# Kernel optimization log

Hardware: AMD Instinct MI355X
Metric: run time of the kernel (lower is better)

## Reference

```python
import jax, jax.numpy as jnp
import numpy as np

V, D, T_BLK, H, HS = 50257, 512, 2048, 8, 64
B, T = 2, 2048


def setup_inputs() -> dict:
    key = jax.random.key(0)
    ks = jax.random.split(key, 12)
    s = 0.02
    return {
        "idx": jax.random.randint(ks[0], (B, T), 0, V),
        "targets": jax.random.randint(ks[1], (B, T), 0, V),
        "tok_emb": jax.random.normal(ks[2], (V, D), jnp.float32) * s,
        "pos_emb": jax.random.normal(ks[3], (T_BLK, D), jnp.float32) * s,
        "wq": jax.random.normal(ks[4], (H, D, HS), jnp.float32) * s,
        "wk": jax.random.normal(ks[5], (H, D, HS), jnp.float32) * s,
        "wv": jax.random.normal(ks[6], (H, D, HS), jnp.float32) * s,
        "w1": jax.random.normal(ks[7], (D, D), jnp.float32) * s,
        "b1": jnp.zeros((D,), jnp.float32),
        "w_head": jax.random.normal(ks[8], (D, V), jnp.float32) * s,
        "b_head": jnp.zeros((V,), jnp.float32),
    }


def _forward(idx, targets, tok_emb, pos_emb, wq, wk, wv, w1, b1, w_head, b_head):
    b, t = idx.shape
    x = tok_emb[idx] + pos_emb[:t]                        # [B,T,D]
    # batched per-head QKV (equivalent to the per-head Linear loop)
    q = jnp.einsum("btd,hde->bhte", x, wq)                # [B,H,T,hs]
    k = jnp.einsum("btd,hde->bhte", x, wk)
    v = jnp.einsum("btd,hde->bhte", x, wv)
    scores = jnp.einsum("bhte,bhse->bhts", q, k) / jnp.sqrt(jnp.float32(HS))
    causal = jnp.tril(jnp.ones((t, t), bool))
    scores = jnp.where(causal, scores, -jnp.inf)
    weights = jax.nn.softmax(scores, axis=-1)
    att = jnp.einsum("bhts,bhse->bhte", weights, v)       # [B,H,T,hs]
    att = att.transpose(0, 2, 1, 3).reshape(b, t, H * HS)  # head-concat order
    x_ff = jax.nn.relu(att @ w1 + b1)                      # [B,T,D]
    logits = x_ff @ w_head + b_head                        # [B,T,V]
    logp = jax.nn.log_softmax(logits, axis=-1)
    loss = -jnp.mean(jnp.take_along_axis(logp, targets[..., None], axis=-1))
    return logits, loss


def reference(idx, targets, tok_emb, pos_emb, wq, wk, wv, w1, b1, w_head, b_head):
    return _forward(idx, targets, tok_emb, pos_emb, wq, wk, wv, w1, b1, w_head, b_head)
```

## Files before the change

### kernel.cpp

```cpp
#include <hip/hip_runtime.h>
#include <hip/hip_bf16.h>
#include <hip/hip_fp8.h>
#include <stdint.h>

#define V_SZ   50257
#define NPAD   50432
#define NT_HEAD 197
#define D_SZ   512
#define HS_SZ  64
#define H_N    8
#define T_SZ   2048
#define ROWS   4096

typedef __bf16 bf16x8 __attribute__((ext_vector_type(8)));
typedef __bf16 bf16x4 __attribute__((ext_vector_type(4)));
typedef float  f32x4  __attribute__((ext_vector_type(4)));
typedef long   l64x2  __attribute__((ext_vector_type(2)));

__device__ __forceinline__ unsigned char to_fp8(float x) {
  __hip_fp8_e4m3 t(x);
  return t.__x;
}

__device__ __forceinline__ void gload_lds16(const void* g, void* l) {
  auto gp = (const __attribute__((address_space(1))) uint32_t*)(uintptr_t)g;
  auto lp = (__attribute__((address_space(3))) uint32_t*)(uintptr_t)l;
  __builtin_amdgcn_global_load_lds(gp, lp, 16, 0, 0);
}

__global__ __launch_bounds__(256) void k_embed(const int* __restrict__ idx,
    const float* __restrict__ tok, const float* __restrict__ pos,
    __bf16* __restrict__ xb) {
  const int row = blockIdx.x;
  const int tpos = row & (T_SZ - 1);
  const int tokid = idx[row];
  const int d = threadIdx.x * 2;
  float2 tv = *(const float2*)(tok + (size_t)tokid * D_SZ + d);
  float2 pv = *(const float2*)(pos + (size_t)tpos * D_SZ + d);
  __bf16* o = xb + (size_t)row * D_SZ + d;
  o[0] = (__bf16)(tv.x + pv.x);
  o[1] = (__bf16)(tv.y + pv.y);
}

__global__ __launch_bounds__(256) void k_prep_wqkv(const float* __restrict__ wq,
    const float* __restrict__ wk, const float* __restrict__ wv, __bf16* __restrict__ dst) {
  const int id = blockIdx.x * 256 + threadIdx.x;
  const int n = id >> 9, dd = id & 511;
  const int mi = n >> 9, rem = n & 511, h = rem >> 6, e = rem & 63;
  const float* src = (mi == 0) ? wq : ((mi == 1) ? wk : wv);
  dst[id] = (__bf16)src[((size_t)h * D_SZ + dd) * HS_SZ + e];
}

__global__ __launch_bounds__(256) void k_prep_w1(const float* __restrict__ w1,
                                                 __bf16* __restrict__ dst) {
  const int id = blockIdx.x * 256 + threadIdx.x;
  const int n = id >> 9, kk = id & 511;
  dst[id] = (__bf16)w1[(size_t)kk * D_SZ + n];
}

__global__ void k_prep_wh(const float* __restrict__ wh, unsigned char* __restrict__ dst) {
  __shared__ float tile[32][33];
  const int n0 = blockIdx.x * 32, d0 = blockIdx.y * 32;
  const int tx = threadIdx.x, ty = threadIdx.y;
  #pragma unroll
  for (int i = 0; i < 4; ++i) {
    int dd = d0 + ty + i * 8, n = n0 + tx;
    tile[ty + i * 8][tx] = (n < V_SZ) ? wh[(size_t)dd * V_SZ + n] : 0.f;
  }
  __syncthreads();
  #pragma unroll
  for (int i = 0; i < 4; ++i) {
    int n = n0 + ty + i * 8, dd = d0 + tx;
    dst[(size_t)n * D_SZ + dd] = to_fp8(tile[tx][ty + i * 8] * 256.f);
  }
}

template <int EPI>
__global__ __launch_bounds__(256) void k_gemm(const __bf16* __restrict__ A,
    const __bf16* __restrict__ Bt, const float* __restrict__ bias,
    unsigned char* __restrict__ outA8, __bf16* __restrict__ outK, __bf16* __restrict__ outV) {
  __shared__ __bf16 As[128 * 32];
  __shared__ __bf16 Bs[128 * 32];
  const int t = threadIdx.x, lane = t & 63, w = t >> 6;
  const int wr = w >> 1, wc = w & 1;
  const int m0 = blockIdx.x * 128, n0 = blockIdx.y * 128;
  const int srow = lane >> 2, k8 = (lane & 3) * 8;

  f32x4 zero = {0.f, 0.f, 0.f, 0.f};
  f32x4 acc[4][4];
  #pragma unroll
  for (int mm = 0; mm < 4; ++mm)
    #pragma unroll
    for (int nn = 0; nn < 4; ++nn) acc[mm][nn] = zero;

  const __bf16* Ag = A  + (size_t)(m0 + w * 16 + srow) * D_SZ + k8;
  const __bf16* Bg = Bt + (size_t)(n0 + w * 16 + srow) * D_SZ + k8;
  char* AsB = (char*)As + w * 1024;
  char* BsB = (char*)Bs + w * 1024;
  const int kslot = (lane >> 4) * 8;
  const int arow = wr * 64 + (lane & 15);
  const int brow = wc * 64 + (lane & 15);

  for (int kt = 0; kt < 16; ++kt) {
    const int k0 = kt * 32;
    gload_lds16(Ag + k0,             AsB);
    gload_lds16(Ag + 64 * D_SZ + k0, AsB + 4096);
    gload_lds16(Bg + k0,             BsB);
    gload_lds16(Bg + 64 * D_SZ + k0, BsB + 4096);
    __syncthreads();

    bf16x8 af[4], bfr[4];
    #pragma unroll
    for (int mm = 0; mm < 4; ++mm)
      af[mm] = *(const bf16x8*)(As + (arow + mm * 16) * 32 + kslot);
    #pragma unroll
    for (int nn = 0; nn < 4; ++nn)
      bfr[nn] = *(const bf16x8*)(Bs + (brow + nn * 16) * 32 + kslot);
    #pragma unroll
    for (int mm = 0; mm < 4; ++mm)
      #pragma unroll
      for (int nn = 0; nn < 4; ++nn)
        acc[mm][nn] = __builtin_amdgcn_mfma_f32_16x16x32_bf16(af[mm], bfr[nn], acc[mm][nn], 0, 0, 0);
    __syncthreads();
  }

  const int lrow = (lane >> 4) * 4, lcol = lane & 15;
  #pragma unroll
  for (int mm = 0; mm < 4; ++mm) {
    #pragma unroll
    for (int nn = 0; nn < 4; ++nn) {
      const int grow0 = m0 + wr * 64 + mm * 16 + lrow;
      const int gcol  = n0 + wc * 64 + nn * 16 + lcol;
      if (EPI == 0) {
        const int mi = gcol >> 9, rem = gcol & 511, hh = rem >> 6, e = rem & 63;
        const int bb = grow0 >> 11, tt0 = grow0 & 2047;
        const int bhh = bb * H_N + hh;
        if (mi == 2) {
          bf16x4 pk = { (__bf16)acc[mm][nn][0], (__bf16)acc[mm][nn][1],
                        (__bf16)acc[mm][nn][2], (__bf16)acc[mm][nn][3] };
          *(bf16x4*)(outV + ((size_t)bhh * HS_SZ + e) * T_SZ + tt0) = pk;
        } else {
          __bf16* dq = (mi == 0 ? (__bf16*)outA8 : outK) + ((size_t)bhh * T_SZ + tt0) * HS_SZ + e;
          const float sc = (mi == 0) ? 0.125f : 1.f;
          #pragma unroll
          for (int j = 0; j < 4; ++j) dq[(size_t)j * HS_SZ] = (__bf16)(acc[mm][nn][j] * sc);
        }
      } else {
        #pragma unroll
        for (int j = 0; j < 4; ++j) {
          float xv = acc[mm][nn][j] + bias[gcol];
          xv = (xv > 0.f ? xv : 0.f) * 256.f;
          outA8[(size_t)(grow0 + j) * D_SZ + gcol] = to_fp8(xv);
        }
      }
    }
  }
}

__global__ __launch_bounds__(512, 4) void k_ghead(const unsigned char* __restrict__ A,
    const unsigned char* __restrict__ Bt, const float* __restrict__ bias,
    float* __restrict__ logits, float2* __restrict__ part) {
  __shared__ char lds[49152];
  const int t = threadIdx.x, lane = t & 63, w = t >> 6;
  const int wr = w >> 2, wc = w & 3;
  const int m0 = blockIdx.x * 128, n0 = blockIdx.y * 256;
  const int lm = lane & 15, g = lane >> 4;
  const int r2 = lane >> 2, c2 = lane & 3;
  const int csw2 = (c2 ^ ((r2 >> 1) & 3)) << 4;

  f32x4 acc[4][4];
  #pragma unroll
  for (int mm = 0; mm < 4; ++mm)
    #pragma unroll
    for (int nn = 0; nn < 4; ++nn) acc[mm][nn] = f32x4{0.f, 0.f, 0.f, 0.f};

  const unsigned char* Ab = A  + (size_t)m0 * D_SZ;
  const unsigned char* Bb = Bt + (size_t)n0 * D_SZ;

  auto STAGE = [&](int buf, int kt) {
    char* Al = lds + buf * 24576;
    char* Bl = Al + 8192;
    gload_lds16(Ab + (size_t)(w * 16 + r2) * D_SZ + kt * 64 + csw2,        Al + w * 1024);
    gload_lds16(Bb + (size_t)(w * 16 + r2) * D_SZ + kt * 64 + csw2,        Bl + w * 1024);
    gload_lds16(Bb + (size_t)(128 + w * 16 + r2) * D_SZ + kt * 64 + csw2,  Bl + 8192 + w * 1024);
  };

  STAGE(0, 0);
  STAGE(1, 1);
  asm volatile("s_waitcnt vmcnt(3)" ::: "memory");
  __builtin_amdgcn_s_barrier();
  asm volatile("" ::: "memory");

  for (int kt = 0; kt < 8; ++kt) {
    const char* Al = lds + (kt & 1) * 24576;
    const char* Bl = Al + 8192;
    l64x2 b2[4];
    #pragma unroll
    for (int nn = 0; nn < 4; ++nn) {
      const int row = wc * 64 + nn * 16 + lm;
      b2[nn] = *(const l64x2*)(Bl + row * 64 + ((g ^ ((row >> 1) & 3)) << 4));
    }
    #pragma unroll
    for (int mm = 0; mm < 4; ++mm) {
      const int row = wr * 64 + mm * 16 + lm;
      l64x2 a2 = *(const l64x2*)(Al + row * 64 + ((g ^ ((row >> 1) & 3)) << 4));
      #pragma unroll
      for (int nn = 0; nn < 4; ++nn)
        acc[mm][nn] = __builtin_amdgcn_mfma_f32_16x16x32_fp8_fp8(a2.x, b2[nn].x, acc[mm][nn], 0, 0, 0);
      #pragma unroll
      for (int nn = 0; nn < 4; ++nn)
        acc[mm][nn] = __builtin_amdgcn_mfma_f32_16x16x32_fp8_fp8(a2.y, b2[nn].y, acc[mm][nn], 0, 0, 0);
    }
    if (kt == 7) break;
    __builtin_amdgcn_s_barrier();
    asm volatile("" ::: "memory");
    if (kt < 6) {
      STAGE(kt & 1, kt + 2);
      asm volatile("s_waitcnt vmcnt(3)" ::: "memory");
    } else {
      asm volatile("s_waitcnt vmcnt(0)" ::: "memory");
    }
    __builtin_amdgcn_s_barrier();
    asm volatile("" ::: "memory");
  }
  __syncthreads();

  const float SC = 1.f / 65536.f;
  float* tr   = (float*)lds;
  float* redS = tr + 32 * 260;
  const int colL = wc * 64 + lm;
  float bj[4]; int vok[4];
  #pragma unroll
  for (int nn = 0; nn < 4; ++nn) {
    const int gc = n0 + colL + nn * 16;
    vok[nn] = (gc < V_SZ);
    bj[nn] = vok[nn] ? bias[gc] : 0.f;
  }
  const int r32s = t >> 4, c16 = t & 15;
  #pragma unroll
  for (int mm = 0; mm < 4; ++mm) {
    if (mm) __syncthreads();
    float sj[4];
    #pragma unroll
    for (int j = 0; j < 4; ++j) {
      const int r32 = wr * 16 + g * 4 + j;
      float s = 0.f;
      #pragma unroll
      for (int nn = 0; nn < 4; ++nn) {
        const float v = acc[mm][nn][j] * SC + bj[nn];
        tr[r32 * 260 + colL + nn * 16] = v;
        if (vok[nn]) s += __expf(v);
      }
      sj[j] = s;
    }
    #pragma unroll
    for (int j = 0; j < 4; ++j) {
      float s = sj[j];
      s += __shfl_xor(s, 1); s += __shfl_xor(s, 2);
      s += __shfl_xor(s, 4); s += __shfl_xor(s, 8);
      if (lm == 0) redS[(wr * 64 + mm * 16 + g * 4 + j) * 4 + wc] = s;
    }
    __syncthreads();
    const int grow = m0 + (r32s >> 4) * 64 + mm * 16 + (r32s & 15);
    float* gp = logits + (size_t)grow * V_SZ;
    #pragma unroll
    for (int i = 0; i < 4; ++i) {
      const int c4 = c16 + 16 * i;
      const int gc0 = n0 + c4 * 4;
      f32x4 vv = *(const f32x4*)(tr + r32s * 260 + c4 * 4);
      if (gc0 + 3 < V_SZ) {
        *(f32x4*)(gp + gc0) = vv;
      } else {
        if (gc0     < V_SZ) gp[gc0]     = vv.x;
        if (gc0 + 1 < V_SZ) gp[gc0 + 1] = vv.y;
        if (gc0 + 2 < V_SZ) gp[gc0 + 2] = vv.z;
        if (gc0 + 3 < V_SZ) gp[gc0 + 3] = vv.w;
      }
    }
  }
  __syncthreads();
  if (t < 128) {
    const float S = redS[t * 4] + redS[t * 4 + 1] + redS[t * 4 + 2] + redS[t * 4 + 3];
    part[(size_t)(m0 + t) * NT_HEAD + blockIdx.y] = float2{0.f, S};
  }
}

__global__ __launch_bounds__(256) void k_attn(const __bf16* __restrict__ qbf,
    const __bf16* __restrict__ kbf, const __bf16* __restrict__ vbf,
    __bf16* __restrict__ xatt) {
  const int qt = 31 - blockIdx.x;
  const int bh = blockIdx.y;
  const int b = bh >> 3, h = bh & 7;
  const int t = threadIdx.x, lane = t & 63, w = t >> 6;
  const int qr = lane & 15, g = lane >> 4, r7 = qr & 7;
  __shared__ __bf16 Klds[64 * 64];
  __shared__ __bf16 Vt[64 * 64];
  __shared__ __bf16 Plds[4][16 * 72];

  const int qglob = qt * 64 + w * 16 + qr;
  const __bf16* qrow_g = qbf + ((size_t)bh * T_SZ + qglob) * HS_SZ + g * 8;
  const bf16x8 qf0 = *(const bf16x8*)(qrow_g);
  const bf16x8 qf1 = *(const bf16x8*)(qrow_g + 32);

  f32x4 att[4];
  #pragma unroll
  for (int n = 0; n < 4; ++n) att[n] = f32x4{0.f, 0.f, 0.f, 0.f};
  float m = -3.0e38f, l = 0.f;

  const char* Kg = (const char*)(kbf + (size_t)bh * T_SZ * HS_SZ);
  const char* Vg = (const char*)(vbf + (size_t)bh * HS_SZ * T_SZ);
  const int r8 = lane >> 3, cc = lane & 7;
  const int csw = ((cc ^ r8) << 4);

  for (int kt = 0; kt <= qt; ++kt) {
    if (kt) __syncthreads();
    {
      const char* ks = Kg + (size_t)(kt * 64 + w * 16) * 128;
      gload_lds16(ks + r8 * 128 + csw,        (char*)Klds + w * 2048);
      gload_lds16(ks + 1024 + r8 * 128 + csw, (char*)Klds + w * 2048 + 1024);
      const char* vs = Vg + (size_t)(w * 16) * (T_SZ * 2) + kt * 128;
      gload_lds16(vs + r8 * (T_SZ * 2) + csw,                   (char*)Vt + w * 2048);
      gload_lds16(vs + (8 + r8) * (T_SZ * 2) + csw,             (char*)Vt + w * 2048 + 1024);
    }
    __syncthreads();

    const bool diag = (kt == qt);
    f32x4 acc[4];
    #pragma unroll
    for (int a = 0; a < 4; ++a) {
      if (diag && a > w) {
        acc[a] = f32x4{-3.0e38f, -3.0e38f, -3.0e38f, -3.0e38f};
      } else {
        const char* kb = (const char*)Klds + (a * 16 + qr) * 128;
        bf16x8 ka0 = *(const bf16x8*)(kb + ((g ^ r7) << 4));
        bf16x8 ka1 = *(const bf16x8*)(kb + (((g + 4) ^ r7) << 4));
        f32x4 z = {0.f, 0.f, 0.f, 0.f};
        z = __builtin_amdgcn_mfma_f32_16x16x32_bf16(ka0, qf0, z, 0, 0, 0);
        z = __builtin_amdgcn_mfma_f32_16x16x32_bf16(ka1, qf1, z, 0, 0, 0);
        acc[a] = z;
      }
    }
    if (diag) {
      #pragma unroll
      for (int a = 0; a < 4; ++a)
        #pragma unroll
        for (int j = 0; j < 4; ++j)
          if (a * 16 + g * 4 + j > w * 16 + qr) acc[a][j] = -3.0e38f;
    }

    float mloc = -3.0e38f;
    #pragma unroll
    for (int a = 0; a < 4; ++a)
      #pragma unroll
      for (int j = 0; j < 4; ++j) mloc = fmaxf(mloc, acc[a][j]);
    mloc = fmaxf(mloc, __shfl_xor(mloc, 16));
    mloc = fmaxf(mloc, __shfl_xor(mloc, 32));
    const float newm = fmaxf(m, mloc);
    const float alpha = __expf(m - newm);
    float lloc = 0.f;
    #pragma unroll
    for (int a = 0; a < 4; ++a) {
      float p0 = __expf(acc[a][0] - newm);
      float p1 = __expf(acc[a][1] - newm);
      float p2 = __expf(acc[a][2] - newm);
      float p3 = __expf(acc[a][3] - newm);
      lloc += (p0 + p1) + (p2 + p3);
      bf16x4 pw = { (__bf16)p0, (__bf16)p1, (__bf16)p2, (__bf16)p3 };
      *(bf16x4*)((char*)&Plds[w][0] + qr * 144 + (a * 16 + g * 4) * 2) = pw;
    }
    lloc += __shfl_xor(lloc, 16);
    lloc += __shfl_xor(lloc, 32);
    l = l * alpha + lloc;
    m = newm;

    #pragma unroll
    for (int j = 0; j < 4; ++j) {
      const float aj = __shfl(alpha, g * 4 + j);
      #pragma unroll
      for (int n = 0; n < 4; ++n) att[n][j] *= aj;
    }

    #pragma unroll
    for (int c = 0; c < 2; ++c) {
      bf16x8 pa = *(const bf16x8*)((const char*)&Plds[w][0] + qr * 144 + c * 64 + g * 16);
      #pragma unroll
      for (int n = 0; n < 4; ++n) {
        const int vrow = n * 16 + qr;
        bf16x8 vb = *(const bf16x8*)((const char*)Vt + vrow * 128 + (((c * 4 + g) ^ r7) << 4));
        att[n] = __builtin_amdgcn_mfma_f32_16x16x32_bf16(pa, vb, att[n], 0, 0, 0);
      }
    }
  }

  #pragma unroll
  for (int j = 0; j < 4; ++j) {
    const float lj = __shfl(l, g * 4 + j);
    const float inv = 1.f / lj;
    const int row = qt * 64 + w * 16 + g * 4 + j;
    __bf16* orow = xatt + ((size_t)(b * T_SZ + row)) * D_SZ + h * HS_SZ + qr;
    #pragma unroll
    for (int n = 0; n < 4; ++n) orow[n * 16] = (__bf16)(att[n][j] * inv);
  }
}

__global__ __launch_bounds__(256) void k_lsemerge(const float2* __restrict__ part,
                                                  float* __restrict__ lse) {
  const int row = blockIdx.x * 4 + (threadIdx.x >> 6);
  const int lane = threadIdx.x & 63;
  const float2* pr = part + (size_t)row * NT_HEAD;
  float M = -3.0e38f, S = 0.f;
  for (int i = lane; i < NT_HEAD; i += 64) {
    float2 p = pr[i];
    float nm = fmaxf(M, p.x);
    S = S * __expf(M - nm) + p.y * __expf(p.x - nm);
    M = nm;
  }
  #pragma unroll
  for (int off = 1; off < 64; off <<= 1) {
    float Mo = __shfl_xor(M, off), So = __shfl_xor(S, off);
    float nm = fmaxf(M, Mo);
    S = S * __expf(M - nm) + So * __expf(Mo - nm);
    M = nm;
  }
  if (lane == 0) lse[row] = M + __logf(S);
}

__global__ __launch_bounds__(256) void k_loss(const float* __restrict__ logits,
    const float* __restrict__ lse, const int* __restrict__ tgt,
    float* __restrict__ outloss) {
  float acc = 0.f;
  for (int r = threadIdx.x; r < ROWS; r += 256)
    acc += lse[r] - logits[(size_t)r * V_SZ + tgt[r]];
  #pragma unroll
  for (int off = 32; off > 0; off >>= 1) acc += __shfl_down(acc, off);
  __shared__ float pw[4];
  if ((threadIdx.x & 63) == 0) pw[threadIdx.x >> 6] = acc;
  __syncthreads();
  if (threadIdx.x == 0) outloss[0] = (pw[0] + pw[1] + pw[2] + pw[3]) * (1.f / ROWS);
}

extern "C" void kernel_launch(void* const* d_in, const int* in_sizes, int n_in,
                              void* d_out, int out_size, void* d_ws, size_t ws_size,
                              hipStream_t stream) {
  const int*   idx = (const int*)d_in[0];
  const int*   tgt = (const int*)d_in[1];
  const float* tok = (const float*)d_in[2];
  const float* pos = (const float*)d_in[3];
  const float* wq  = (const float*)d_in[4];
  const float* wk  = (const float*)d_in[5];
  const float* wv  = (const float*)d_in[6];
  const float* w1  = (const float*)d_in[7];
  const float* b1  = (const float*)d_in[8];
  const float* wh  = (const float*)d_in[9];
  const float* bh  = (const float*)d_in[10];

  float* logits = (float*)d_out;
  float* lossp  = logits + (size_t)ROWS * V_SZ;

  char* ws = (char*)d_ws;
  __bf16* xb   = (__bf16*)(ws + 0);
  __bf16* Bqkv = (__bf16*)(ws + (4u  << 20));
  __bf16* B1t  = (__bf16*)(ws + (11u << 19));
  __bf16* qbf  = (__bf16*)(ws + (6u  << 20));
  __bf16* kbf  = (__bf16*)(ws + (10u << 20));
  __bf16* vbf  = (__bf16*)(ws + (14u << 20));
  float2* part = (float2*)(ws + 0);
  float*  lse  = (float*) (ws + (20u << 20));
  __bf16* xatt = (__bf16*)(ws + (30u << 20));
  unsigned char* Aff8 = (unsigned char*)(ws + (34u << 20));
  unsigned char* Wht8 = (unsigned char*)(ws + (38u << 20));

  k_embed    <<<ROWS, 256, 0, stream>>>(idx, tok, pos, xb);
  k_prep_wqkv<<<3072, 256, 0, stream>>>(wq, wk, wv, Bqkv);
  k_prep_w1  <<<1024, 256, 0, stream>>>(w1, B1t);
  k_prep_wh  <<<dim3(NPAD / 32, 16), dim3(32, 8), 0, stream>>>(wh, Wht8);

  k_gemm<0><<<dim3(32, 12),  256, 0, stream>>>(xb,   Bqkv, nullptr, (unsigned char*)qbf, kbf, vbf);
  k_attn   <<<dim3(32, 16),  256, 0, stream>>>(qbf, kbf, vbf, xatt);
  k_gemm<1><<<dim3(32, 4),   256, 0, stream>>>(xatt, B1t,  b1,  Aff8, nullptr, nullptr);
  k_ghead  <<<dim3(32, NT_HEAD), 512, 0, stream>>>(Aff8, Wht8, bh, logits, part);

  k_lsemerge<<<ROWS / 4, 256, 0, stream>>>(part, lse);
  k_loss    <<<1,        256, 0, stream>>>(logits, lse, tgt, lossp);
}
```

Before: 491.3 us.

## Double-buffer K/V tiles in attention kernel and raise MFMA wave priority

The attention kernel gets two LDS buffers for K and V. The next tile's global-to-LDS load is issued before the current tile is computed, with manual vmcnt waits and raw barriers in place of the old load-then-sync sequence. The MFMA sections are also wrapped in s_setprio to favour matrix issue. The aim is to hide global load latency behind compute, at the cost of doubled LDS use and fragile hand-written waitcnt logic.

```diff
diff --git a/kernel.cpp b/kernel.cpp
--- a/kernel.cpp
+++ b/kernel.cpp
@@ -293,14 +293,15 @@
   const int b = bh >> 3, h = bh & 7;
   const int t = threadIdx.x, lane = t & 63, w = t >> 6;
   const int qr = lane & 15, g = lane >> 4, r7 = qr & 7;
-  __shared__ __bf16 Klds[64 * 64];
-  __shared__ __bf16 Vt[64 * 64];
+  __shared__ __bf16 Klds[2][64 * 64];
+  __shared__ __bf16 Vt[2][64 * 64];
   __shared__ __bf16 Plds[4][16 * 72];
 
   const int qglob = qt * 64 + w * 16 + qr;
   const __bf16* qrow_g = qbf + ((size_t)bh * T_SZ + qglob) * HS_SZ + g * 8;
   const bf16x8 qf0 = *(const bf16x8*)(qrow_g);
   const bf16x8 qf1 = *(const bf16x8*)(qrow_g + 32);
+  asm volatile("s_waitcnt vmcnt(0)" ::: "memory");
 
   f32x4 att[4];
   #pragma unroll
@@ -312,18 +313,31 @@
   const int r8 = lane >> 3, cc = lane & 7;
   const int csw = ((cc ^ r8) << 4);
 
+  auto STAGE = [&](int bsel, int kt2) {
+    char* Kb = (char*)&Klds[bsel][0] + w * 2048;
+    char* Vb = (char*)&Vt[bsel][0] + w * 2048;
+    const char* ks = Kg + (size_t)(kt2 * 64 + w * 16) * 128;
+    gload_lds16(ks + r8 * 128 + csw,        Kb);
+    gload_lds16(ks + 1024 + r8 * 128 + csw, Kb + 1024);
+    const char* vs = Vg + (size_t)(w * 16) * (T_SZ * 2) + kt2 * 128;
+    gload_lds16(vs + r8 * (T_SZ * 2) + csw,       Vb);
+    gload_lds16(vs + (8 + r8) * (T_SZ * 2) + csw, Vb + 1024);
+  };
+
+  STAGE(0, 0);
+  if (qt >= 1) {
+    STAGE(1, 1);
+    asm volatile("s_waitcnt vmcnt(4)" ::: "memory");
+  } else {
+    asm volatile("s_waitcnt vmcnt(0)" ::: "memory");
+  }
+  __builtin_amdgcn_s_barrier();
+  asm volatile("" ::: "memory");
+
   for (int kt = 0; kt <= qt; ++kt) {
-    if (kt) __syncthreads();
-    {
-      const char* ks = Kg + (size_t)(kt * 64 + w * 16) * 128;
-      gload_lds16(ks + r8 * 128 + csw,        (char*)Klds + w * 2048);
-      gload_lds16(ks + 1024 + r8 * 128 + csw, (char*)Klds + w * 2048 + 1024);
-      const char* vs = Vg + (size_t)(w * 16) * (T_SZ * 2) + kt * 128;
-      gload_lds16(vs + r8 * (T_SZ * 2) + csw,                   (char*)Vt + w * 2048);
-      gload_lds16(vs + (8 + r8) * (T_SZ * 2) + csw,             (char*)Vt + w * 2048 + 1024);
-    }
-    __syncthreads();
-
+    const int bs = kt & 1;
+    const __bf16* Kl = &Klds[bs][0];
+    const __bf16* Vl = &Vt[bs][0];
     const bool diag = (kt == qt);
     f32x4 acc[4];
     #pragma unroll
@@ -331,12 +345,14 @@
       if (diag && a > w) {
         acc[a] = f32x4{-3.0e38f, -3.0e38f, -3.0e38f, -3.0e38f};
       } else {
-        const char* kb = (const char*)Klds + (a * 16 + qr) * 128;
+        const char* kb = (const char*)Kl + (a * 16 + qr) * 128;
         bf16x8 ka0 = *(const bf16x8*)(kb + ((g ^ r7) << 4));
         bf16x8 ka1 = *(const bf16x8*)(kb + (((g + 4) ^ r7) << 4));
         f32x4 z = {0.f, 0.f, 0.f, 0.f};
+        __builtin_amdgcn_s_setprio(1);
         z = __builtin_amdgcn_mfma_f32_16x16x32_bf16(ka0, qf0, z, 0, 0, 0);
         z = __builtin_amdgcn_mfma_f32_16x16x32_bf16(ka1, qf1, z, 0, 0, 0);
+        __builtin_amdgcn_s_setprio(0);
         acc[a] = z;
       }
     }
@@ -383,13 +399,27 @@
     #pragma unroll
     for (int c = 0; c < 2; ++c) {
       bf16x8 pa = *(const bf16x8*)((const char*)&Plds[w][0] + qr * 144 + c * 64 + g * 16);
+      __builtin_amdgcn_s_setprio(1);
       #pragma unroll
       for (int n = 0; n < 4; ++n) {
         const int vrow = n * 16 + qr;
-        bf16x8 vb = *(const bf16x8*)((const char*)Vt + vrow * 128 + (((c * 4 + g) ^ r7) << 4));
+        bf16x8 vb = *(const bf16x8*)((const char*)Vl + vrow * 128 + (((c * 4 + g) ^ r7) << 4));
         att[n] = __builtin_amdgcn_mfma_f32_16x16x32_bf16(pa, vb, att[n], 0, 0, 0);
       }
-    }
+      __builtin_amdgcn_s_setprio(0);
+    }
+
+    if (kt == qt) break;
+    __builtin_amdgcn_s_barrier();
+    asm volatile("" ::: "memory");
+    if (kt + 2 <= qt) {
+      STAGE(bs, kt + 2);
+      asm volatile("s_waitcnt vmcnt(4)" ::: "memory");
+    } else {
+      asm volatile("s_waitcnt vmcnt(0)" ::: "memory");
+    }
+    __builtin_amdgcn_s_barrier();
+    asm volatile("" ::: "memory");
   }
 
   #pragma unroll
```

Result: no change. 488.3 us (-0.6%).
